# Optimization experiments

Measured on AMD Instinct MI355X. Metric: run time of the kernel, lower is better.

Reference implementation:

```python
import jax, jax.numpy as jnp
import numpy as np

CLASSES = 21
IOU_THRESH = 0.5
ALPHA = 0.25   # focal loss alpha
GAMMA = 2.0    # focal loss gamma
SL1_BETA = 1.0 # torch SmoothL1Loss default beta
CLS_W = 1.0
REG_W = 1.0
NUM_ANCHORS = 98304
NUM_TARGETS = 1024


def _compute_iou(boxes_a, boxes_b):
    # boxes_a: [T,4], boxes_b: [A,4] in (x1,y1,x2,y2) -> [T,A]
    lt = jnp.maximum(boxes_a[:, None, :2], boxes_b[None, :, :2])
    rb = jnp.minimum(boxes_a[:, None, 2:], boxes_b[None, :, 2:])
    wh = jnp.clip(rb - lt, 0.0)
    inter = wh[..., 0] * wh[..., 1]
    area_a = (boxes_a[:, 2] - boxes_a[:, 0]) * (boxes_a[:, 3] - boxes_a[:, 1])
    area_b = (boxes_b[:, 2] - boxes_b[:, 0]) * (boxes_b[:, 3] - boxes_b[:, 1])
    union = area_a[:, None] + area_b[None, :] - inter
    return inter / jnp.maximum(union, 1e-8)


def _encode(boxes, anchors):
    bw = boxes[:, 2] - boxes[:, 0]
    bh = boxes[:, 3] - boxes[:, 1]
    bcx = boxes[:, 0] + 0.5 * bw
    bcy = boxes[:, 1] + 0.5 * bh
    aw = anchors[:, 2] - anchors[:, 0]
    ah = anchors[:, 3] - anchors[:, 1]
    acx = anchors[:, 0] + 0.5 * aw
    acy = anchors[:, 1] + 0.5 * ah
    tx = (bcx - acx) / aw
    ty = (bcy - acy) / ah
    tw = jnp.log(jnp.maximum(bw, 1e-8) / aw)
    th = jnp.log(jnp.maximum(bh, 1e-8) / ah)
    return jnp.stack([tx, ty, tw, th], axis=1)


def _focal_loss(logits, targets):
    # elementwise sigmoid focal loss (no reduction)
    p = jax.nn.sigmoid(logits)
    # numerically stable BCE with logits
    ce = jnp.maximum(logits, 0.0) - logits * targets + jnp.log1p(jnp.exp(-jnp.abs(logits)))
    p_t = p * targets + (1.0 - p) * (1.0 - targets)
    alpha_t = ALPHA * targets + (1.0 - ALPHA) * (1.0 - targets)
    return alpha_t * (1.0 - p_t) ** GAMMA * ce


def _smooth_l1(diff):
    ad = jnp.abs(diff)
    return jnp.where(ad < SL1_BETA, 0.5 * diff * diff / SL1_BETA, ad - 0.5 * SL1_BETA)


def setup_inputs() -> dict:
    key = jax.random.key(0)
    kA, kW, kT, kJ, kL, kC, kB = jax.random.split(key, 7)
    A, T = NUM_ANCHORS, NUM_TARGETS
    centers = jax.random.uniform(kA, (A, 2), minval=0.15, maxval=0.85)
    sizes = jax.random.uniform(kW, (A, 2), minval=0.05, maxval=0.30)
    anchors = jnp.concatenate([centers - 0.5 * sizes, centers + 0.5 * sizes], axis=1)
    # targets = jittered anchors so IoU >= 0.5 matches exist
    idx = jax.random.randint(kT, (T,), 0, A)
    jitter = jax.random.uniform(kJ, (T, 4), minval=-0.01, maxval=0.01)
    target_boxes = anchors[idx] + jitter
    target_labels = jax.random.randint(kL, (T,), 0, CLASSES)
    classification_preds = jax.random.normal(kC, (A, CLASSES), dtype=jnp.float32)
    boxes_preds = jax.random.normal(kB, (A, 4), dtype=jnp.float32)
    return {
        'classification_preds': classification_preds,
        'boxes_preds': boxes_preds,
        'anchors': anchors,
        'target_boxes': target_boxes,
        'target_labels': target_labels,
    }


def reference(classification_preds, boxes_preds, anchors, target_boxes, target_labels):
    iou = _compute_iou(target_boxes, anchors)  # [T, A]

    # anchor-side matching -> classification targets
    max_iou_for_anchors = jnp.max(iou, axis=0)          # [A]
    target_ids_for_anchors = jnp.argmax(iou, axis=0)     # [A]
    positive_mask = max_iou_for_anchors >= IOU_THRESH    # [A] bool
    n_pos = jnp.sum(positive_mask.astype(jnp.float32))
    onehot = jax.nn.one_hot(target_labels[target_ids_for_anchors], CLASSES, dtype=jnp.float32)
    cls_targets = jnp.where(positive_mask[:, None], onehot, 0.0)
    cls_loss = jnp.sum(_focal_loss(classification_preds, cls_targets)) / n_pos

    max_iou_for_targets = jnp.max(iou, axis=1)          # [T]
    anchor_ids_for_targets = jnp.argmax(iou, axis=1)     # [T]
    t_mask = (max_iou_for_targets >= IOU_THRESH).astype(jnp.float32)  # [T]
    matched_anchors = anchors[anchor_ids_for_targets]    # [T,4]
    encoded = _encode(target_boxes, matched_anchors)     # [T,4]
    pred = boxes_preds[anchor_ids_for_targets]           # [T,4]
    diff = (pred - encoded) * t_mask[:, None]
    n_match = jnp.maximum(jnp.sum(t_mask), 1.0)
    reg_loss = jnp.sum(_smooth_l1(diff)) / (n_match * 4.0)  # mean over matched elements

    w_cls = cls_loss * CLS_W
    w_reg = reg_loss * REG_W
    return (w_cls + w_reg, w_cls, w_reg)
```

## Files before the change

kernel.cpp:

```cpp
#include <hip/hip_runtime.h>
#include <stdint.h>

#define NA 98304
#define NT 1024
#define NC 21
#define ACH 192
#define TCH 8
#define NBLK (ACH * TCH)
#define HI_MIN 0xBF000000u


__device__ __forceinline__ float f0(float x) {
    const float ax = fabsf(x);
    const float u  = __expf(-ax);
    const float ce = fmaxf(x, 0.f) + __logf(1.f + u);
    const float p  = (x >= 0.f ? 1.f : u) / (1.f + u);
    return 0.75f * p * p * ce;
}
__device__ __forceinline__ float f1(float x) {
    const float ax = fabsf(x);
    const float u  = __expf(-ax);
    const float ce = fmaxf(x, 0.f) - x + __logf(1.f + u);
    const float p  = (x >= 0.f ? 1.f : u) / (1.f + u);
    const float q  = 1.f - p;
    return 0.25f * q * q * ce;
}
__device__ __forceinline__ unsigned long long mk_key(float iou, unsigned int idx) {
    return ((unsigned long long)(__float_as_uint(iou) | 0x80000000u) << 32) |
           (unsigned long long)(0xFFFFFFFFu - idx);
}
__device__ __forceinline__ float smooth_l1(float d) {
    const float ad = fabsf(d);
    return (ad < 1.f) ? 0.5f * d * d : ad - 0.5f;
}

__global__ __launch_bounds__(256) void k_all(
    const float* __restrict__ preds,
    const float4* __restrict__ preds4,
    const int* __restrict__ tlabels,
    const float4* __restrict__ anchors,
    const float4* __restrict__ tboxes,
    const float4* __restrict__ bpreds,
    unsigned long long* __restrict__ akeys,
    unsigned long long* __restrict__ tkeys,
    float* __restrict__ f0_part,
    float* __restrict__ corr_part,
    int* __restrict__ npos_part,
    int* __restrict__ done_ac,
    int* __restrict__ done2,
    float* __restrict__ out)
{
    __shared__ float4 s_t[128];
    __shared__ unsigned long long s_tk[128];
    __shared__ float s_f[4];
    __shared__ int   s_last, s_fin;
    __shared__ float s_a[4];
    __shared__ int   s_c[4];
    __shared__ double s_d[4];
    __shared__ int    s_i[4];
    __shared__ float  s_s[4], s_m[4];

    const int tid   = threadIdx.x;
    const int ac    = blockIdx.x;
    const int L     = blockIdx.y * ACH + ac;
    const int tbase = blockIdx.y * 128;
    const int a0    = ac * 512 + tid;
    const int a1    = a0 + 256;
    const int lane  = tid & 63, wid = tid >> 6;

    if (tid < 128) {
        s_t[tid]  = tboxes[tbase + tid];
        s_tk[tid] = 0ull;
    }
    const float4 A0 = anchors[a0];
    const float4 A1 = anchors[a1];

    float facc;
    {
        const int pb = L * 336;
        const float4 v0 = preds4[pb + tid];
        facc = (f0(v0.x) + f0(v0.y)) + (f0(v0.z) + f0(v0.w));
        if (tid < 80) {
            const float4 v1 = preds4[pb + 256 + tid];
            facc += (f0(v1.x) + f0(v1.y)) + (f0(v1.z) + f0(v1.w));
        }
    }
    __syncthreads();

    const float ar0 = (A0.z - A0.x) * (A0.w - A0.y);
    const float ar1 = (A1.z - A1.x) * (A1.w - A1.y);

    float b0 = 0.f, b1 = 0.f;
    int   i0 = -1,  i1 = -1;

    #pragma unroll 4
    for (int t = 0; t < 128; ++t) {
        const float4 tb = s_t[t];
        const float sa = (tb.z - tb.x) * (tb.w - tb.y);
        {
            const float lx = fmaxf(A0.x, tb.x);
            const float ly = fmaxf(A0.y, tb.y);
            const float rx = fminf(A0.z, tb.z);
            const float ry = fminf(A0.w, tb.w);
            const float w  = fmaxf(rx - lx, 0.f);
            const float h  = fmaxf(ry - ly, 0.f);
            const float inter = w * h;
            const float uni = (ar0 + sa) - inter;
            if (__builtin_expect(inter + inter >= uni, 0)) {
                const float iou = inter / uni;
                if (iou > b0) { b0 = iou; i0 = t; }
                atomicMax(&s_tk[t], mk_key(iou, (unsigned int)a0));
            }
        }
        {
            const float lx = fmaxf(A1.x, tb.x);
            const float ly = fmaxf(A1.y, tb.y);
            const float rx = fminf(A1.z, tb.z);
            const float ry = fminf(A1.w, tb.w);
            const float w  = fmaxf(rx - lx, 0.f);
            const float h  = fmaxf(ry - ly, 0.f);
            const float inter = w * h;
            const float uni = (ar1 + sa) - inter;
            if (__builtin_expect(inter + inter >= uni, 0)) {
                const float iou = inter / uni;
                if (iou > b1) { b1 = iou; i1 = t; }
                atomicMax(&s_tk[t], mk_key(iou, (unsigned int)a1));
            }
        }
    }

    if (i0 >= 0) atomicMax(&akeys[a0], mk_key(b0, (unsigned int)(tbase + i0)));
    if (i1 >= 0) atomicMax(&akeys[a1], mk_key(b1, (unsigned int)(tbase + i1)));

    for (int o = 32; o > 0; o >>= 1) facc += __shfl_down(facc, o);
    if (lane == 0) s_f[wid] = facc;

    __syncthreads();
    if (tid < 128) {
        const unsigned long long tk = s_tk[tid];
        if (tk != 0ull) atomicMax(&tkeys[tbase + tid], tk);
    }
    if (tid == 0)
        atomicExch(&f0_part[L], s_f[0] + s_f[1] + s_f[2] + s_f[3]);

    __syncthreads();
    if (tid == 0) {
        __threadfence();
        s_last = (atomicAdd(&done_ac[ac], 1) == TCH - 1);
    }
    __syncthreads();
    if (!s_last) return;

    float acc = 0.f;
    int   cnt = 0;
    {
        const unsigned long long k = atomicMax(&akeys[a0], 0ull);
        if ((unsigned int)(k >> 32) >= HI_MIN) {
            cnt = 1;
            const int lab = tlabels[0xFFFFFFFFu - (unsigned int)k];
            const float x = preds[a0 * NC + lab];
            acc += f1(x) - f0(x);
        }
    }
    {
        const unsigned long long k = atomicMax(&akeys[a1], 0ull);
        if ((unsigned int)(k >> 32) >= HI_MIN) {
            cnt += 1;
            const int lab = tlabels[0xFFFFFFFFu - (unsigned int)k];
            const float x = preds[a1 * NC + lab];
            acc += f1(x) - f0(x);
        }
    }
    if (tid < TCH) acc += atomicAdd(&f0_part[ac + tid * ACH], 0.f);

    for (int o = 32; o > 0; o >>= 1) {
        acc += __shfl_down(acc, o);
        cnt += __shfl_down(cnt, o);
    }
    if (lane == 0) { s_a[wid] = acc; s_c[wid] = cnt; }
    __syncthreads();
    if (tid == 0) {
        atomicExch(&corr_part[ac], s_a[0] + s_a[1] + s_a[2] + s_a[3]);
        atomicExch(&npos_part[ac], s_c[0] + s_c[1] + s_c[2] + s_c[3]);
        __threadfence();
        s_fin = (atomicAdd(done2, 1) == ACH - 1);
    }
    __syncthreads();
    if (!s_fin) return;

    double cl = 0.0;
    int    np = 0;
    if (tid < ACH) {
        cl = (double)atomicAdd(&corr_part[tid], 0.f);
        np = atomicAdd(&npos_part[tid], 0);
    }
    float s = 0.f, m = 0.f;
    #pragma unroll
    for (int j = 0; j < 4; ++j) {
        const int t = tid + 256 * j;
        const unsigned long long key = atomicMax(&tkeys[t], 0ull);
        if ((unsigned int)(key >> 32) >= HI_MIN) {
            const unsigned int ga = 0xFFFFFFFFu - (unsigned int)key;
            const float4 tb  = tboxes[t];
            const float4 abx = anchors[ga];
            const float4 pb  = bpreds[ga];
            const float bw = tb.z - tb.x, bh = tb.w - tb.y;
            const float bcx = tb.x + 0.5f * bw, bcy = tb.y + 0.5f * bh;
            const float aw = abx.z - abx.x, ah = abx.w - abx.y;
            const float acx = abx.x + 0.5f * aw, acy = abx.y + 0.5f * ah;
            const float tx = (bcx - acx) / aw;
            const float ty = (bcy - acy) / ah;
            const float tw = logf(fmaxf(bw, 1e-8f) / aw);
            const float th = logf(fmaxf(bh, 1e-8f) / ah);
            s += smooth_l1(pb.x - tx) + smooth_l1(pb.y - ty) +
                 smooth_l1(pb.z - tw) + smooth_l1(pb.w - th);
            m += 1.f;
        }
    }
    for (int o = 32; o > 0; o >>= 1) {
        cl += __shfl_down(cl, o);
        np += __shfl_down(np, o);
        s  += __shfl_down(s, o);
        m  += __shfl_down(m, o);
    }
    __syncthreads();
    if (lane == 0) { s_d[wid] = cl; s_i[wid] = np; s_s[wid] = s; s_m[wid] = m; }
    __syncthreads();
    if (tid == 0) {
        const double cls_sum = s_d[0] + s_d[1] + s_d[2] + s_d[3];
        const int    npos    = s_i[0] + s_i[1] + s_i[2] + s_i[3];
        const float  rs      = s_s[0] + s_s[1] + s_s[2] + s_s[3];
        const float  rm      = s_m[0] + s_m[1] + s_m[2] + s_m[3];
        const float cls = (float)(cls_sum / (double)npos);
        const float reg = rs / (fmaxf(rm, 1.f) * 4.f);
        out[0] = cls + reg;
        out[1] = cls;
        out[2] = reg;
    }
}

extern "C" void kernel_launch(void* const* d_in, const int* in_sizes, int n_in,
                              void* d_out, int out_size, void* d_ws, size_t ws_size,
                              hipStream_t stream) {
    const float*  preds   = (const float*)d_in[0];
    const float4* preds4  = (const float4*)d_in[0];
    const float4* bpreds  = (const float4*)d_in[1];
    const float4* anchors = (const float4*)d_in[2];
    const float4* tboxes  = (const float4*)d_in[3];
    const int*    tlabels = (const int*)d_in[4];

    char* ws = (char*)d_ws;
    int*    done2     = (int*)(ws + 0);
    int*    done_ac   = (int*)(ws + 64);
    float*  f0_part   = (float*)(ws + 1024);
    float*  corr_part = (float*)(ws + 7168);
    int*    npos_part = (int*)(ws + 7936);
    unsigned long long* tkeys = (unsigned long long*)(ws + 12288);
    unsigned long long* akeys = (unsigned long long*)(ws + 20480);

    hipMemsetAsync(d_ws, 0, 1024, stream);

    k_all<<<dim3(ACH, TCH), 256, 0, stream>>>(
        preds, preds4, tlabels, anchors, tboxes, bpreds,
        akeys, tkeys, f0_part, corr_part, npos_part,
        done_ac, done2, (float*)d_out);
}
```

Baseline: 137.5 us.

## Split targets into 16 chunks per anchor block and use relaxed atomic loads

Doubles the grid along the target dimension so each block handles 64 targets instead of 128, which doubles block count for better occupancy and latency hiding, and halves the per-block focal-loss slice. Target areas are precomputed into shared memory once. Read-modify-write atomics used as loads are replaced by relaxed agent-scope atomic loads and stores plus explicit acquire fences. The trade-off is twice as many per-anchor global atomicMax updates and more blocks contending on the done counters.

```diff
diff --git a/kernel.cpp b/kernel.cpp
--- a/kernel.cpp
+++ b/kernel.cpp
@@ -5,7 +5,7 @@
 #define NT 1024
 #define NC 21
 #define ACH 192
-#define TCH 8
+#define TCH 16
 #define NBLK (ACH * TCH)
 #define HI_MIN 0xBF000000u
 
@@ -32,6 +32,15 @@
 __device__ __forceinline__ float smooth_l1(float d) {
     const float ad = fabsf(d);
     return (ad < 1.f) ? 0.5f * d * d : ad - 0.5f;
+}
+__device__ __forceinline__ unsigned long long aload64(const unsigned long long* p) {
+    return __hip_atomic_load(p, __ATOMIC_RELAXED, __HIP_MEMORY_SCOPE_AGENT);
+}
+__device__ __forceinline__ float aloadf(const float* p) {
+    return __hip_atomic_load(p, __ATOMIC_RELAXED, __HIP_MEMORY_SCOPE_AGENT);
+}
+__device__ __forceinline__ int aloadi(const int* p) {
+    return __hip_atomic_load(p, __ATOMIC_RELAXED, __HIP_MEMORY_SCOPE_AGENT);
 }
 
 __global__ __launch_bounds__(256) void k_all(
@@ -50,8 +59,9 @@
     int* __restrict__ done2,
     float* __restrict__ out)
 {
-    __shared__ float4 s_t[128];
-    __shared__ unsigned long long s_tk[128];
+    __shared__ float4 s_t[64];
+    __shared__ float  s_sa[64];
+    __shared__ unsigned long long s_tk[64];
     __shared__ float s_f[4];
     __shared__ int   s_last, s_fin;
     __shared__ float s_a[4];
@@ -63,27 +73,24 @@
     const int tid   = threadIdx.x;
     const int ac    = blockIdx.x;
     const int L     = blockIdx.y * ACH + ac;
-    const int tbase = blockIdx.y * 128;
+    const int tbase = blockIdx.y * 64;
     const int a0    = ac * 512 + tid;
     const int a1    = a0 + 256;
     const int lane  = tid & 63, wid = tid >> 6;
 
-    if (tid < 128) {
-        s_t[tid]  = tboxes[tbase + tid];
+    if (tid < 64) {
+        const float4 tb = tboxes[tbase + tid];
+        s_t[tid]  = tb;
+        s_sa[tid] = (tb.z - tb.x) * (tb.w - tb.y);
         s_tk[tid] = 0ull;
     }
     const float4 A0 = anchors[a0];
     const float4 A1 = anchors[a1];
 
-    float facc;
-    {
-        const int pb = L * 336;
-        const float4 v0 = preds4[pb + tid];
+    float facc = 0.f;
+    if (tid < 168) {
+        const float4 v0 = preds4[L * 168 + tid];
         facc = (f0(v0.x) + f0(v0.y)) + (f0(v0.z) + f0(v0.w));
-        if (tid < 80) {
-            const float4 v1 = preds4[pb + 256 + tid];
-            facc += (f0(v1.x) + f0(v1.y)) + (f0(v1.z) + f0(v1.w));
-        }
     }
     __syncthreads();
 
@@ -94,9 +101,9 @@
     int   i0 = -1,  i1 = -1;
 
     #pragma unroll 4
-    for (int t = 0; t < 128; ++t) {
+    for (int t = 0; t < 64; ++t) {
         const float4 tb = s_t[t];
-        const float sa = (tb.z - tb.x) * (tb.w - tb.y);
+        const float  sa = s_sa[t];
         {
             const float lx = fmaxf(A0.x, tb.x);
             const float ly = fmaxf(A0.y, tb.y);
@@ -136,12 +143,13 @@
     if (lane == 0) s_f[wid] = facc;
 
     __syncthreads();
-    if (tid < 128) {
+    if (tid < 64) {
         const unsigned long long tk = s_tk[tid];
         if (tk != 0ull) atomicMax(&tkeys[tbase + tid], tk);
     }
     if (tid == 0)
-        atomicExch(&f0_part[L], s_f[0] + s_f[1] + s_f[2] + s_f[3]);
+        __hip_atomic_store(&f0_part[L], s_f[0] + s_f[1] + s_f[2] + s_f[3],
+                           __ATOMIC_RELAXED, __HIP_MEMORY_SCOPE_AGENT);
 
     __syncthreads();
     if (tid == 0) {
@@ -150,11 +158,12 @@
     }
     __syncthreads();
     if (!s_last) return;
+    __builtin_amdgcn_fence(__ATOMIC_ACQUIRE, "agent");
 
     float acc = 0.f;
     int   cnt = 0;
     {
-        const unsigned long long k = atomicMax(&akeys[a0], 0ull);
+        const unsigned long long k = aload64(&akeys[a0]);
         if ((unsigned int)(k >> 32) >= HI_MIN) {
             cnt = 1;
             const int lab = tlabels[0xFFFFFFFFu - (unsigned int)k];
@@ -163,7 +172,7 @@
         }
     }
     {
-        const unsigned long long k = atomicMax(&akeys[a1], 0ull);
+        const unsigned long long k = aload64(&akeys[a1]);
         if ((unsigned int)(k >> 32) >= HI_MIN) {
             cnt += 1;
             const int lab = tlabels[0xFFFFFFFFu - (unsigned int)k];
@@ -171,7 +180,7 @@
             acc += f1(x) - f0(x);
         }
     }
-    if (tid < TCH) acc += atomicAdd(&f0_part[ac + tid * ACH], 0.f);
+    if (tid < TCH) acc += aloadf(&f0_part[ac + tid * ACH]);
 
     for (int o = 32; o > 0; o >>= 1) {
         acc += __shfl_down(acc, o);
@@ -180,25 +189,28 @@
     if (lane == 0) { s_a[wid] = acc; s_c[wid] = cnt; }
     __syncthreads();
     if (tid == 0) {
-        atomicExch(&corr_part[ac], s_a[0] + s_a[1] + s_a[2] + s_a[3]);
-        atomicExch(&npos_part[ac], s_c[0] + s_c[1] + s_c[2] + s_c[3]);
+        __hip_atomic_store(&corr_part[ac], s_a[0] + s_a[1] + s_a[2] + s_a[3],
+                           __ATOMIC_RELAXED, __HIP_MEMORY_SCOPE_AGENT);
+        __hip_atomic_store(&npos_part[ac], s_c[0] + s_c[1] + s_c[2] + s_c[3],
+                           __ATOMIC_RELAXED, __HIP_MEMORY_SCOPE_AGENT);
         __threadfence();
         s_fin = (atomicAdd(done2, 1) == ACH - 1);
     }
     __syncthreads();
     if (!s_fin) return;
+    __builtin_amdgcn_fence(__ATOMIC_ACQUIRE, "agent");
 
     double cl = 0.0;
     int    np = 0;
     if (tid < ACH) {
-        cl = (double)atomicAdd(&corr_part[tid], 0.f);
-        np = atomicAdd(&npos_part[tid], 0);
+        cl = (double)aloadf(&corr_part[tid]);
+        np = aloadi(&npos_part[tid]);
     }
     float s = 0.f, m = 0.f;
     #pragma unroll
     for (int j = 0; j < 4; ++j) {
         const int t = tid + 256 * j;
-        const unsigned long long key = atomicMax(&tkeys[t], 0ull);
+        const unsigned long long key = aload64(&tkeys[t]);
         if ((unsigned int)(key >> 32) >= HI_MIN) {
             const unsigned int ga = 0xFFFFFFFFu - (unsigned int)key;
             const float4 tb  = tboxes[t];
@@ -253,10 +265,10 @@
     int*    done2     = (int*)(ws + 0);
     int*    done_ac   = (int*)(ws + 64);
     float*  f0_part   = (float*)(ws + 1024);
-    float*  corr_part = (float*)(ws + 7168);
-    int*    npos_part = (int*)(ws + 7936);
-    unsigned long long* tkeys = (unsigned long long*)(ws + 12288);
-    unsigned long long* akeys = (unsigned long long*)(ws + 20480);
+    float*  corr_part = (float*)(ws + 13312);
+    int*    npos_part = (int*)(ws + 14080);
+    unsigned long long* tkeys = (unsigned long long*)(ws + 16384);
+    unsigned long long* akeys = (unsigned long long*)(ws + 24576);
 
     hipMemsetAsync(d_ws, 0, 1024, stream);
 
```

After: 155.6 us. 1.13x slower.
